# Kernel tuning notes

Hardware: AMD Instinct MI355X
Metric: run time of the kernel (lower is better)

The kernel has to match this reference:

```python
import jax, jax.numpy as jnp
import numpy as np

BETA = 4.0  # temperature of soft cluster assignment in filling loss


def _pairwise_sq_dist(a, b):
    # a: [N,D], b: [K,D] -> [N,K] squared euclidean distances
    return (jnp.sum(a * a, -1, keepdims=True)
            - 2.0 * (a @ b.T)
            + jnp.sum(b * b, -1)[None, :])


def setup_inputs() -> dict:
    key = jax.random.key(0)
    k1, k2, k3, k4 = jax.random.split(key, 4)
    N, D, K = 131072, 64, 16
    x = jax.random.normal(k1, (N, D), jnp.float32)
    cluster_centers = jax.random.normal(k2, (K, D), jnp.float32)
    target = jax.random.normal(k3, (N, D), jnp.float32)
    ft = jax.random.uniform(k4, (K,), jnp.float32)
    filling_target = ft / ft.sum()
    # prediction = kmeans assignment of the fixed target set (computed once, constant)
    prediction = jnp.argmin(_pairwise_sq_dist(target, cluster_centers), axis=-1)
    return {"x": x, "cluster_centers": cluster_centers,
            "filling_target": filling_target, "target": target,
            "prediction": prediction}


def reference(x, cluster_centers, filling_target, target, prediction):
    N, D = x.shape
    Nt = target.shape[0]
    K = cluster_centers.shape[0]
    BIG = jnp.finfo(x.dtype).max  # padding value that sorts to the end

    d2 = _pairwise_sq_dist(x, cluster_centers)  # [N,K]

    # --- cluster filling MSE: soft assignment fractions vs filling_target ---
    soft = jax.nn.softmax(-BETA * d2, axis=-1)          # [N,K]
    filling = soft.mean(axis=0)                          # [K]
    loss_fil = jnp.mean((filling - filling_target) ** 2)

    # --- per-cluster sorted (per-dimension 1D) Wasserstein distance ---
    pred_x = jax.lax.stop_gradient(jnp.argmin(d2, axis=-1))  # kmeans_predict(x).detach()
    L = min(N, Nt)  # static upper bound on per-cluster min_size
    rows = jnp.arange(L)

    loss_med = jnp.zeros((), x.dtype)
    for k in range(K):  # fixed structural loop over clusters
        mx = pred_x == k
        mt = prediction == k
        m = jnp.minimum(mx.sum(), mt.sum())  # min_size (dynamic value, static shapes)
        # keep only the FIRST m members (original order), as x[in_cluster][:m]
        keep_x = mx & ((jnp.cumsum(mx) - 1) < m)
        keep_t = mt & ((jnp.cumsum(mt) - 1) < m)
        # mask out non-members with BIG so they sort to the bottom, sort per dim
        xs = jnp.sort(jnp.where(keep_x[:, None], x, BIG), axis=0)[:L]       # [L,D]
        ts = jnp.sort(jnp.where(keep_t[:, None], target, BIG), axis=0)[:L]  # [L,D]
        valid = (rows < m)[:, None]                                          # [L,1]
        diff = jnp.where(valid, jnp.abs(xs - ts), 0.0)
        # mean(|sort(x) - sort(y)|) over the m x D selected elements
        denom = (m * D).astype(x.dtype)
        loss_med = loss_med + jnp.where(m > 0, diff.sum() / denom, 0.0)

    return loss_fil + loss_med
```

## Files before the change

### kernel.cpp

```cpp
#include <hip/hip_runtime.h>
#include <stdint.h>

#define N_ROWS 131072
#define DIMS 64
#define KCL 16
#define BETA 4.0f
#define NBLK 512
#define LCH 8192
#define LST 512
#define SEG_STRIDE 263168
#define VOFF (1u<<21)

typedef unsigned long long u64;
typedef unsigned int u32;

__device__ __forceinline__ u32 enc_f(float f) {
  u32 u = __float_as_uint(f);
  return (u & 0x80000000u) ? ~u : (u | 0x80000000u);
}
__device__ __forceinline__ float dec_f(u32 e) {
  u32 u = (e & 0x80000000u) ? (e & 0x7FFFFFFFu) : ~e;
  return __uint_as_float(u);
}
__device__ __forceinline__ u32 U4(u32 u) { return u ^ ((u >> 3) & 7u); }

#define CS(a,b,dd) { u32 _mn = min(a,b), _mx = max(a,b); a = (dd)?_mn:_mx; b = (dd)?_mx:_mn; }
#define CSV(A,B,D) { CS(A.x,B.x,D) CS(A.y,B.y,D) CS(A.z,B.z,D) CS(A.w,B.w,D) }

#define M16G(a,b,c,d,e,f,g,h,i2,j2,k2,l,m,n,o,p,D) \
  CS(a,i2,D) CS(b,j2,D) CS(c,k2,D) CS(d,l,D) CS(e,m,D) CS(f,n,D) CS(g,o,D) CS(h,p,D) \
  CS(a,e,D)  CS(b,f,D)  CS(c,g,D)  CS(d,h,D) CS(i2,m,D) CS(j2,n,D) CS(k2,o,D) CS(l,p,D) \
  CS(a,c,D)  CS(b,d,D)  CS(e,g,D)  CS(f,h,D) CS(i2,k2,D) CS(j2,l,D) CS(m,o,D) CS(n,p,D) \
  CS(a,b,D)  CS(c,d,D)  CS(e,f,D)  CS(g,h,D) CS(i2,j2,D) CS(k2,l,D) CS(m,n,D) CS(o,p,D)

#define SORT16G(a,b,c,d,e,f,g,h,i2,j2,k2,l,m,n,o,p,D) \
  CS(a,b,D) CS(c,d,!(D)) CS(e,f,D) CS(g,h,!(D)) CS(i2,j2,D) CS(k2,l,!(D)) CS(m,n,D) CS(o,p,!(D)) \
  CS(a,c,D) CS(b,d,D) CS(e,g,!(D)) CS(f,h,!(D)) CS(i2,k2,D) CS(j2,l,D) CS(m,o,!(D)) CS(n,p,!(D)) \
  CS(a,b,D) CS(c,d,D) CS(e,f,!(D)) CS(g,h,!(D)) CS(i2,j2,D) CS(k2,l,D) CS(m,n,!(D)) CS(o,p,!(D)) \
  CS(a,e,D) CS(b,f,D) CS(c,g,D) CS(d,h,D) CS(i2,m,!(D)) CS(j2,n,!(D)) CS(k2,o,!(D)) CS(l,p,!(D)) \
  CS(a,c,D) CS(b,d,D) CS(e,g,D) CS(f,h,D) CS(i2,k2,!(D)) CS(j2,l,!(D)) CS(m,o,!(D)) CS(n,p,!(D)) \
  CS(a,b,D) CS(c,d,D) CS(e,f,D) CS(g,h,D) CS(i2,j2,!(D)) CS(k2,l,!(D)) CS(m,n,!(D)) CS(o,p,!(D)) \
  M16G(a,b,c,d,e,f,g,h,i2,j2,k2,l,m,n,o,p,D)

#define MERGE16F(D) M16G(r0,r1,r2,r3,r4,r5,r6,r7,r8,r9,r10,r11,r12,r13,r14,r15,D)
#define SORT16F(D)  SORT16G(r0,r1,r2,r3,r4,r5,r6,r7,r8,r9,r10,r11,r12,r13,r14,r15,D)

#define LOADTILE16(src) \
  { uint4 _a0=src[U4(ub+0)],_a1=src[U4(ub+1)],_a2=src[U4(ub+2)],_a3=src[U4(ub+3)]; \
    r0=_a0.x;r1=_a0.y;r2=_a0.z;r3=_a0.w; r4=_a1.x;r5=_a1.y;r6=_a1.z;r7=_a1.w; \
    r8=_a2.x;r9=_a2.y;r10=_a2.z;r11=_a2.w; r12=_a3.x;r13=_a3.y;r14=_a3.z;r15=_a3.w; }

#define STORETILE16(dst) \
  { dst[U4(ub+0)]=make_uint4(r0,r1,r2,r3);   dst[U4(ub+1)]=make_uint4(r4,r5,r6,r7); \
    dst[U4(ub+2)]=make_uint4(r8,r9,r10,r11); dst[U4(ub+3)]=make_uint4(r12,r13,r14,r15); }

__device__ __forceinline__ void wave_tail(uint4* lds4, u32 RU, u32 Lw, u32 gbase,
                                          u32 k, u32 jtop, u32 lane)
{
  u32 j = jtop;
  while (j >= 32u) {
    u32 ud = j >> 3;
    if (lane < (Lw >> 4)) {
      u32 bu = RU + (((lane & ~(ud - 1u)) << 2) | (lane & (ud - 1u)));
      bool up = (((gbase + (bu << 2)) & k) == 0u);
      uint4 A0 = lds4[U4(bu)],           A1 = lds4[U4(bu + ud)],
            A2 = lds4[U4(bu + 2u * ud)], A3 = lds4[U4(bu + 3u * ud)];
      CSV(A0,A2,up) CSV(A1,A3,up)
      CSV(A0,A1,up) CSV(A2,A3,up)
      lds4[U4(bu)] = A0;           lds4[U4(bu + ud)] = A1;
      lds4[U4(bu + 2u * ud)] = A2; lds4[U4(bu + 3u * ud)] = A3;
    }
    j >>= 2;
  }
  if (j == 16u) {
    u32 total = Lw >> 3;
    for (u32 inst = lane; inst < total; inst += 64u) {
      u32 bu = RU + (((inst & ~3u) << 1) | (inst & 3u));
      bool up = (((gbase + (bu << 2)) & k) == 0u);
      uint4 A = lds4[U4(bu)], B = lds4[U4(bu + 4u)];
      CSV(A,B,up)
      lds4[U4(bu)] = A; lds4[U4(bu + 4u)] = B;
    }
  }
}

__device__ __forceinline__ void block_cross(uint4* lds4, u32 Wn, u32 gbase,
                                            u32 k, u32 jtop, u32 tid)
{
  if (jtop == 1024u) {
    u32 total = Wn >> 3;
    for (u32 inst = tid; inst < total; inst += LST) {
      u32 bu = ((inst & ~255u) << 1) | (inst & 255u);
      bool up = (((gbase + (bu << 2)) & k) == 0u);
      uint4 A = lds4[U4(bu)], B = lds4[U4(bu + 256u)];
      CSV(A,B,up)
      lds4[U4(bu)] = A; lds4[U4(bu + 256u)] = B;
    }
  } else if (jtop == 2048u) {
    u32 total = Wn >> 4;
    for (u32 inst = tid; inst < total; inst += LST) {
      u32 bu = ((inst & ~255u) << 2) | (inst & 255u);
      bool up = (((gbase + (bu << 2)) & k) == 0u);
      uint4 A0 = lds4[U4(bu)],         A1 = lds4[U4(bu + 256u)],
            A2 = lds4[U4(bu + 512u)],  A3 = lds4[U4(bu + 768u)];
      CSV(A0,A2,up) CSV(A1,A3,up)
      CSV(A0,A1,up) CSV(A2,A3,up)
      lds4[U4(bu)] = A0;        lds4[U4(bu + 256u)] = A1;
      lds4[U4(bu + 512u)] = A2; lds4[U4(bu + 768u)] = A3;
    }
  } else {
    u32 total = Wn >> 5;
    for (u32 inst = tid; inst < total; inst += LST) {
      u32 bu = ((inst & ~255u) << 3) | (inst & 255u);
      bool up = (((gbase + (bu << 2)) & k) == 0u);
      uint4 A0 = lds4[U4(bu)],          A1 = lds4[U4(bu + 256u)],
            A2 = lds4[U4(bu + 512u)],   A3 = lds4[U4(bu + 768u)],
            A4 = lds4[U4(bu + 1024u)],  A5 = lds4[U4(bu + 1280u)],
            A6 = lds4[U4(bu + 1536u)],  A7 = lds4[U4(bu + 1792u)];
      CSV(A0,A4,up) CSV(A1,A5,up) CSV(A2,A6,up) CSV(A3,A7,up)
      CSV(A0,A2,up) CSV(A1,A3,up) CSV(A4,A6,up) CSV(A5,A7,up)
      CSV(A0,A1,up) CSV(A2,A3,up) CSV(A4,A5,up) CSV(A6,A7,up)
      lds4[U4(bu)] = A0;         lds4[U4(bu + 256u)] = A1;
      lds4[U4(bu + 512u)] = A2;  lds4[U4(bu + 768u)] = A3;
      lds4[U4(bu + 1024u)] = A4; lds4[U4(bu + 1280u)] = A5;
      lds4[U4(bu + 1536u)] = A6; lds4[U4(bu + 1792u)] = A7;
    }
  }
}

__global__ __launch_bounds__(256) void k_assign(
    const float* __restrict__ x, const float* __restrict__ centers,
    const int* __restrict__ predT, int* __restrict__ predX,
    float* __restrict__ fill_sum, u32* __restrict__ histX, u32* __restrict__ histT)
{
  __shared__ float c[KCL][DIMS];
  __shared__ float cn[KCL];
  __shared__ float fs[KCL];
  __shared__ u32 hx[KCL], ht[KCL];
  int tid = threadIdx.x;
  for (int t = tid; t < KCL * DIMS; t += 256) c[t / DIMS][t % DIMS] = centers[t];
  if (tid < KCL) { fs[tid] = 0.f; hx[tid] = 0; ht[tid] = 0; }
  __syncthreads();
  if (tid < KCL) {
    float s = 0.f;
    for (int d = 0; d < DIMS; ++d) s += c[tid][d] * c[tid][d];
    cn[tid] = s;
  }
  __syncthreads();
  int i = blockIdx.x * 256 + tid;
  const float4* xr = (const float4*)(x + (size_t)i * DIMS);
  float dot[KCL];
#pragma unroll
  for (int k = 0; k < KCL; ++k) dot[k] = 0.f;
  for (int t = 0; t < DIMS / 4; ++t) {
    float4 v = xr[t];
#pragma unroll
    for (int k = 0; k < KCL; ++k)
      dot[k] += v.x * c[k][4 * t] + v.y * c[k][4 * t + 1] + v.z * c[k][4 * t + 2] + v.w * c[k][4 * t + 3];
  }
  float sc[KCL];
  float smin = 3.0e38f; int kmin = 0;
#pragma unroll
  for (int k = 0; k < KCL; ++k) {
    sc[k] = cn[k] - 2.f * dot[k];
    if (sc[k] < smin) { smin = sc[k]; kmin = k; }
  }
  float e[KCL]; float esum = 0.f;
#pragma unroll
  for (int k = 0; k < KCL; ++k) { e[k] = expf(-BETA * (sc[k] - smin)); esum += e[k]; }
  float inv = 1.f / esum;
#pragma unroll
  for (int k = 0; k < KCL; ++k) atomicAdd(&fs[k], e[k] * inv);
  predX[i] = kmin;
  atomicAdd(&hx[kmin], 1u);
  atomicAdd(&ht[predT[i]], 1u);
  __syncthreads();
  if (tid < KCL) {
    histX[blockIdx.x * KCL + tid] = hx[tid];
    histT[blockIdx.x * KCL + tid] = ht[tid];
    atomicAdd(&fill_sum[tid], fs[tid]);
  }
}

__global__ __launch_bounds__(512) void k_scan(
    const u32* __restrict__ histX, const u32* __restrict__ histT,
    u32* __restrict__ baseX, u32* __restrict__ baseT,
    const float* __restrict__ fill_sum, const float* __restrict__ ftarget,
    int* __restrict__ m_out, float* __restrict__ w_out,
    int* __restrict__ p_out, int* __restrict__ pOff_out, int* __restrict__ padOff_out,
    int* __restrict__ nlo_out, float* __restrict__ loss_fil)
{
  __shared__ u32 part[2][KCL][17];
  __shared__ u32 tot[2][KCL];
  __shared__ float sq[KCL];
  __shared__ int sp[KCL];
  __shared__ int smv[KCL];
  int tid = threadIdx.x;
  int side = tid >> 8;
  int rem = tid & 255;
  int c = rem >> 4;
  int sub = rem & 15;
  const u32* hist = side ? histT : histX;
  u32* base = side ? baseT : baseX;
  int b0 = sub * 32;
  u32 s = 0;
  for (int b = b0; b < b0 + 32; ++b) s += hist[b * KCL + c];
  part[side][c][sub] = s;
  __syncthreads();
  if (sub == 0) {
    u32 run = 0;
    for (int t = 0; t < 16; ++t) { u32 v = part[side][c][t]; part[side][c][t] = run; run += v; }
    tot[side][c] = run;
  }
  __syncthreads();
  u32 run = part[side][c][sub];
  for (int b = b0; b < b0 + 32; ++b) { base[b * KCL + c] = run; run += hist[b * KCL + c]; }
  if (tid < KCL) {
    int m = min((int)tot[0][tid], (int)tot[1][tid]);
    m_out[tid] = m;
    smv[tid] = m;
    w_out[tid] = (m > 0) ? 1.f / ((float)m * (float)DIMS) : 0.f;
    int pp = 32;
    while (pp < m) pp <<= 1;
    sp[tid] = pp;
    p_out[tid] = pp;
    int nlo = 0;
    if (pp > LCH) {
      int nch = pp / LCH;
      for (int j = 1; j < nch; j += 2) {
        int v = m - j * LCH;
        if (v < 0) v = 0;
        if (v > LCH) v = LCH;
        nlo += LCH - v;
      }
    }
    nlo_out[tid] = nlo;
    float d = fill_sum[tid] / (float)N_ROWS - ftarget[tid];
    sq[tid] = d * d;
  }
  __syncthreads();
  if (tid == 0) {
    float s2 = 0.f;
    int acc = 0, pacc = 0;
    for (int k = 0; k < KCL; ++k) {
      s2 += sq[k];
      pOff_out[k] = acc;
      acc += sp[k];
      padOff_out[k] = pacc;
      pacc += sp[k] - smv[k];
    }
    pOff_out[KCL] = acc;
    padOff_out[KCL] = pacc;
    *loss_fil = s2 / (float)KCL;
  }
}

__global__ __launch_bounds__(256) void k_rank(
    const int* __restrict__ predX, const int* __restrict__ predT,
    const u32* __restrict__ baseX, const u32* __restrict__ baseT,
    const int* __restrict__ m, int* __restrict__ rankX, int* __restrict__ rankT)
{
  __shared__ int wcX[4][KCL], wcT[4][KCL];
  int tid = threadIdx.x;
  int lane = tid & 63, wave = tid >> 6;
  int i = blockIdx.x * 256 + tid;
  int kx = predX[i], kt = predT[i];
  u64 below = (1ull << lane) - 1ull;
  int lrX = 0, lrT = 0;
  for (int cc = 0; cc < KCL; ++cc) {
    u64 mx = __ballot(kx == cc);
    u64 mt = __ballot(kt == cc);
    if (kx == cc) lrX = __popcll(mx & below);
    if (kt == cc) lrT = __popcll(mt & below);
    if (lane == 0) { wcX[wave][cc] = __popcll(mx); wcT[wave][cc] = __popcll(mt); }
  }
  __syncthreads();
  int wbX = 0, wbT = 0;
  for (int w2 = 0; w2 < wave; ++w2) { wbX += wcX[w2][kx]; wbT += wcT[w2][kt]; }
  int rX = (int)baseX[blockIdx.x * KCL + kx] + wbX + lrX;
  int rT = (int)baseT[blockIdx.x * KCL + kt] + wbT + lrT;
  rankX[i] = (rX < m[kx]) ? rX : -1;
  rankT[i] = (rT < m[kt]) ? rT : -1;
}

__global__ __launch_bounds__(256) void k_pad(
    u32* __restrict__ vbase, const int* __restrict__ pOffG,
    const int* __restrict__ padOffG, const int* __restrict__ mG,
    const int* __restrict__ pG)
{
  __shared__ int sOff[KCL];
  __shared__ int sPad[KCL + 1];
  __shared__ int sM[KCL];
  __shared__ int sP[KCL];
  int tid = threadIdx.x;
  if (tid < KCL) { sOff[tid] = pOffG[tid]; sM[tid] = mG[tid]; sP[tid] = pG[tid]; }
  if (tid <= KCL) sPad[tid] = padOffG[tid];
  __syncthreads();
  int tot = sPad[KCL];
  u32* seg = vbase + (size_t)blockIdx.y * SEG_STRIDE;
  for (int tt = blockIdx.x * 256 + tid; tt < tot; tt += gridDim.x * 256) {
    int c = 0;
#pragma unroll
    for (int cc = 1; cc < KCL; ++cc) c += (tt >= sPad[cc]) ? 1 : 0;
    int local = sM[c] + (tt - sPad[c]);
    u32 val = (sP[c] > LCH && ((local >> 13) & 1)) ? 0u : 0xFFFFFFFFu;
    seg[sOff[c] + local] = val;
  }
}

__global__ __launch_bounds__(256) void k_scatter(
    const float* __restrict__ x, const float* __restrict__ tgt,
    const int* __restrict__ predX, const int* __restrict__ predT,
    const int* __restrict__ rankX, const int* __restrict__ rankT,
    const int* __restrict__ pOffG,
    u32* __restrict__ valX, u32* __restrict__ valT, int d0, int Dbc)
{
  __shared__ int spOff[KCL + 1];
  int tid = threadIdx.x;
  if (tid <= KCL) spOff[tid] = pOffG[tid];
  __syncthreads();
  int i = blockIdx.x * 256 + tid;
  int cx = predX[i], rx = rankX[i];
  int ct = predT[i], rt = rankT[i];
  bool vec = ((Dbc & 3) == 0);
  if (rx >= 0) {
    size_t pos = (size_t)spOff[cx] + rx;
    const float* xr = x + (size_t)i * DIMS + d0;
    if (vec) {
      const float4* x4 = (const float4*)xr;
      for (int d = 0; d < Dbc; d += 4) {
        float4 v = x4[d >> 2];
        valX[(size_t)(d + 0) * SEG_STRIDE + pos] = enc_f(v.x);
        valX[(size_t)(d + 1) * SEG_STRIDE + pos] = enc_f(v.y);
        valX[(size_t)(d + 2) * SEG_STRIDE + pos] = enc_f(v.z);
        valX[(size_t)(d + 3) * SEG_STRIDE + pos] = enc_f(v.w);
      }
    } else {
      for (int d = 0; d < Dbc; ++d) valX[(size_t)d * SEG_STRIDE + pos] = enc_f(xr[d]);
    }
  }
  if (rt >= 0) {
    size_t pos = (size_t)spOff[ct] + rt;
    const float* tr = tgt + (size_t)i * DIMS + d0;
    if (vec) {
      const float4* t4 = (const float4*)tr;
      for (int d = 0; d < Dbc; d += 4) {
        float4 v = t4[d >> 2];
        valT[(size_t)(d + 0) * SEG_STRIDE + pos] = enc_f(v.x);
        valT[(size_t)(d + 1) * SEG_STRIDE + pos] = enc_f(v.y);
        valT[(size_t)(d + 2) * SEG_STRIDE + pos] = enc_f(v.z);
        valT[(size_t)(d + 3) * SEG_STRIDE + pos] = enc_f(v.w);
      }
    } else {
      for (int d = 0; d < Dbc; ++d) valT[(size_t)d * SEG_STRIDE + pos] = enc_f(tr[d]);
    }
  }
}

__global__ __launch_bounds__(LST, 8) void k_local_sort(
    u32* __restrict__ vbase, const int* __restrict__ pG, const int* __restrict__ pOffG,
    const int* __restrict__ mG)
{
  __shared__ __align__(16) u32 lds[LCH];
  uint4* lds4 = (uint4*)lds;
  int t = blockIdx.x, c = -1, sub = 0, acc = 0;
  for (int cc = 0; cc < KCL; ++cc) {
    int pc0 = pG[cc];
    int nc = (pc0 > LCH) ? (pc0 / LCH) : 1;
    if (t < acc + nc) { c = cc; sub = t - acc; break; }
    acc += nc;
  }
  if (c < 0) return;
  int pc = pG[c];
  u32 CH = (u32)min(pc, LCH);
  u32 gb = (u32)sub * (u32)LCH;
  int v = mG[c] - (int)gb;
  if (v > (int)CH) v = (int)CH;
  if (v <= 0) return;
  u32 W = 32u;
  while (W < (u32)v) W <<= 1;
  if (W > CH) W = CH;
  bool desc = (pc > LCH) && (sub & 1);
  u32 inv = desc ? 0xFFFFFFFFu : 0u;
  u32* seg = vbase + (size_t)blockIdx.y * SEG_STRIDE + pOffG[c] + gb;
  uint4* gp4 = (uint4*)seg;
  u32 tid = threadIdx.x;
  u32 lane = tid & 63u;
  u32 wv = tid >> 6;
  u32 ub = tid << 2;
  u32 bas = tid << 4;
  bool act = (bas < W);
  u32 RU = wv << 8;
  u32 runBase = wv << 10;
  bool wact = (runBase < W);
  u32 Lw = W - runBase; if (Lw > 1024u) Lw = 1024u;
  u32 r0,r1,r2,r3,r4,r5,r6,r7,r8,r9,r10,r11,r12,r13,r14,r15;

  if (act) {
    uint4 a0 = gp4[ub + 0], a1 = gp4[ub + 1], a2 = gp4[ub + 2], a3 = gp4[ub + 3];
    r0 = a0.x^inv; r1 = a0.y^inv; r2  = a0.z^inv; r3  = a0.w^inv;
    r4 = a1.x^inv; r5 = a1.y^inv; r6  = a1.z^inv; r7  = a1.w^inv;
    r8 = a2.x^inv; r9 = a2.y^inv; r10 = a2.z^inv; r11 = a2.w^inv;
    r12 = a3.x^inv; r13 = a3.y^inv; r14 = a3.z^inv; r15 = a3.w^inv;
    bool D = ((bas & 16u) == 0u);
    SORT16F(D);
    STORETILE16(lds4);
  }
  if (wact) {
    for (u32 k = 32u; k <= Lw; k <<= 1) {
      wave_tail(lds4, RU, Lw, 0u, k, k >> 1, lane);
      if (act) {
        LOADTILE16(lds4);
        bool D = ((bas & k) == 0u);
        MERGE16F(D);
        if (k < W) { STORETILE16(lds4); }
        else {
          gp4[ub + 0] = make_uint4(r0^inv, r1^inv, r2^inv, r3^inv);
          gp4[ub + 1] = make_uint4(r4^inv, r5^inv, r6^inv, r7^inv);
          gp4[ub + 2] = make_uint4(r8^inv, r9^inv, r10^inv, r11^inv);
          gp4[ub + 3] = make_uint4(r12^inv, r13^inv, r14^inv, r15^inv);
        }
      }
    }
  }

  if (W >= 2048u) {
    __syncthreads();
    for (u32 k = 2048u; k <= W; k <<= 1) {
      block_cross(lds4, W, 0u, k, k >> 1, tid);
      __syncthreads();
      if (wact) {
        wave_tail(lds4, RU, Lw, 0u, k, 512u, lane);
        if (act) {
          LOADTILE16(lds4);
          bool D = ((bas & k) == 0u);
          MERGE16F(D);
          if (k < W) { STORETILE16(lds4); }
          else {
            gp4[ub + 0] = make_uint4(r0^inv, r1^inv, r2^inv, r3^inv);
            gp4[ub + 1] = make_uint4(r4^inv, r5^inv, r6^inv, r7^inv);
            gp4[ub + 2] = make_uint4(r8^inv, r9^inv, r10^inv, r11^inv);
            gp4[ub + 3] = make_uint4(r12^inv, r13^inv, r14^inv, r15^inv);
          }
        }
      }
      if (k < W) __syncthreads();
    }
  }
}

__global__ __launch_bounds__(256) void k_gpass(
    u32* __restrict__ vbase, const int* __restrict__ pG, const int* __restrict__ pOffG,
    int kk, int j)
{
  u32* base = vbase + (size_t)blockIdx.y * SEG_STRIDE;
  int pb[KCL]; int tot = 0;
#pragma unroll
  for (int c = 0; c < KCL; ++c) {
    pb[c] = tot;
    int pc = pG[c];
    if (pc >= kk) tot += pc >> 1;
  }
  for (int g4 = (blockIdx.x * 256 + threadIdx.x) << 2; g4 < tot; g4 += gridDim.x * 256 * 4) {
    int c = 0;
#pragma unroll
    for (int cc = 1; cc < KCL; ++cc) c += (g4 >= pb[cc]) ? 1 : 0;
    int u = g4 - pb[c];
    int i = ((u & ~(j - 1)) << 1) | (u & (j - 1));
    bool up = ((i & kk) == 0);
    u32* s2 = base + pOffG[c];
    uint4 A = *(const uint4*)(s2 + i);
    uint4 B = *(const uint4*)(s2 + i + j);
    CS(A.x, B.x, up) CS(A.y, B.y, up) CS(A.z, B.z, up) CS(A.w, B.w, up)
    *(uint4*)(s2 + i) = A;
    *(uint4*)(s2 + i + j) = B;
  }
}

__global__ __launch_bounds__(LST, 8) void k_gfinish(
    u32* __restrict__ vbase, const int* __restrict__ pG, const int* __restrict__ pOffG, int kk)
{
  __shared__ __align__(16) u32 lds[LCH];
  uint4* lds4 = (uint4*)lds;
  int t = blockIdx.x, c = -1, sub = 0, acc = 0;
  for (int cc = 0; cc < KCL; ++cc) {
    int pc = pG[cc];
    if (pc < kk) continue;
    int nc = pc / LCH;
    if (t < acc + nc) { c = cc; sub = t - acc; break; }
    acc += nc;
  }
  if (c < 0) return;
  u32 gb = (u32)sub * (u32)LCH;
  u32* seg = vbase + (size_t)blockIdx.y * SEG_STRIDE + pOffG[c] + gb;
  uint4* gp4 = (uint4*)seg;
  u32 tid = threadIdx.x;
  u32 lane = tid & 63u;
  u32 wv = tid >> 6;
  u32 RU = wv << 8;
  u32 ub = tid << 2;
  u32 bas = tid << 4;
  u32 r0,r1,r2,r3,r4,r5,r6,r7,r8,r9,r10,r11,r12,r13,r14,r15;

  for (u32 uu = tid; uu < LCH / 4; uu += LST) lds4[U4(uu)] = gp4[uu];
  __syncthreads();
  block_cross(lds4, (u32)LCH, gb, (u32)kk, 4096u, tid);
  __syncthreads();
  wave_tail(lds4, RU, 1024u, gb, (u32)kk, 512u, lane);
  {
    LOADTILE16(lds4);
    bool up = (((gb + bas) & (u32)kk) == 0u);
    MERGE16F(up);
    gp4[ub + 0] = make_uint4(r0, r1, r2, r3);
    gp4[ub + 1] = make_uint4(r4, r5, r6, r7);
    gp4[ub + 2] = make_uint4(r8, r9, r10, r11);
    gp4[ub + 3] = make_uint4(r12, r13, r14, r15);
  }
}

__global__ __launch_bounds__(256) void k_reduce(
    const u32* __restrict__ valX, const u32* __restrict__ valT,
    const int* __restrict__ pOffG, const int* __restrict__ mG,
    const int* __restrict__ nloG,
    const float* __restrict__ wG, float* __restrict__ lossAcc, int Dbc)
{
  __shared__ int spOff[KCL + 1];
  __shared__ int sm[KCL];
  __shared__ int snlo[KCL];
  __shared__ float swt[KCL];
  __shared__ float red[256];
  int tid = threadIdx.x;
  if (tid <= KCL) spOff[tid] = pOffG[tid];
  if (tid < KCL) { sm[tid] = mG[tid]; snlo[tid] = nloG[tid]; swt[tid] = wG[tid]; }
  __syncthreads();
  int d = blockIdx.y;
  const u32* vx = valX + (size_t)d * SEG_STRIDE;
  const u32* vt = valT + (size_t)d * SEG_STRIDE;
  int P16 = spOff[KCL];
  float s = 0.f;
  for (int pos = blockIdx.x * 256 + tid; pos < P16; pos += gridDim.x * 256) {
    int c = 0;
#pragma unroll
    for (int cc = 1; cc < KCL; ++cc) c += (pos >= spOff[cc]) ? 1 : 0;
    int rel = pos - spOff[c] - snlo[c];
    if ((unsigned)rel < (unsigned)sm[c]) {
      float a = dec_f(vx[pos]), b = dec_f(vt[pos]);
      s += fabsf(a - b) * swt[c];
    }
  }
  red[tid] = s;
  __syncthreads();
  for (int st = 128; st > 0; st >>= 1) {
    if (tid < st) red[tid] += red[tid + st];
    __syncthreads();
  }
  if (tid == 0) atomicAdd(lossAcc, red[0]);
}

__global__ void k_final(const float* __restrict__ lossAcc, const float* __restrict__ loss_fil,
                        float* __restrict__ out)
{
  out[0] = *lossAcc + *loss_fil;
}

extern "C" void kernel_launch(void* const* d_in, const int* in_sizes, int n_in,
                              void* d_out, int out_size, void* d_ws, size_t ws_size,
                              hipStream_t stream)
{
  const float* x       = (const float*)d_in[0];
  const float* centers = (const float*)d_in[1];
  const float* ftarget = (const float*)d_in[2];
  const float* tgt     = (const float*)d_in[3];
  const int*   predT   = (const int*)d_in[4];
  float* out = (float*)d_out;

  char* ws = (char*)d_ws;
  float* fill_sum = (float*)(ws + 0);
  float* lossAcc  = (float*)(ws + 64);
  float* loss_fil = (float*)(ws + 68);
  int*   m_buf    = (int*)(ws + 128);
  float* w_buf    = (float*)(ws + 192);
  int*   p_buf    = (int*)(ws + 256);
  int*   pOff     = (int*)(ws + 320);
  int*   padOff   = (int*)(ws + 400);
  u32* histX = (u32*)(ws + 512);
  u32* histT = (u32*)(ws + 512 + 32768);
  u32* baseX = (u32*)(ws + 512 + 65536);
  u32* baseT = (u32*)(ws + 512 + 98304);
  int* predX = (int*)(ws + 131584);
  int* rankX = (int*)(ws + 655872);
  int* rankT = (int*)(ws + 1180160);
  int* nlo_buf = (int*)(ws + 1704448);
  u32* vbase = (u32*)(ws + VOFF);

  size_t avail_elems = (ws_size > VOFF) ? ((ws_size - VOFF) / 4) : 0;
  int Db = (int)(avail_elems / (2ull * SEG_STRIDE));
  if (Db > DIMS) Db = DIMS;
  if (Db >= 4) Db &= ~3;
  if (Db < 1) Db = 1;

  hipMemsetAsync(ws, 0, 128, stream);
  k_assign<<<NBLK, 256, 0, stream>>>(x, centers, predT, predX, fill_sum, histX, histT);
  k_scan<<<1, 512, 0, stream>>>(histX, histT, baseX, baseT, fill_sum, ftarget,
                                m_buf, w_buf, p_buf, pOff, padOff, nlo_buf, loss_fil);
  k_rank<<<NBLK, 256, 0, stream>>>(predX, predT, baseX, baseT, m_buf, rankX, rankT);

  for (int d0 = 0; d0 < DIMS; d0 += Db) {
    int Dbc = (Db < DIMS - d0) ? Db : (DIMS - d0);
    u32* valX = vbase;
    u32* valT = vbase + (size_t)Dbc * SEG_STRIDE;
    k_pad<<<dim3(16, 2 * Dbc), 256, 0, stream>>>(vbase, pOff, padOff, m_buf, p_buf);
    k_scatter<<<NBLK, 256, 0, stream>>>(x, tgt, predX, predT, rankX, rankT, pOff,
                                        valX, valT, d0, Dbc);
    k_local_sort<<<dim3(40, 2 * Dbc), LST, 0, stream>>>(vbase, p_buf, pOff, m_buf);
    for (int kk = 2 * LCH; kk <= N_ROWS; kk <<= 1) {
      int gx = (kk == 2 * LCH) ? 32 : 8;
      for (int j = kk >> 1; j >= LCH; j >>= 1)
        k_gpass<<<dim3(gx, 2 * Dbc), 256, 0, stream>>>(vbase, p_buf, pOff, kk, j);
      k_gfinish<<<dim3(32, 2 * Dbc), LST, 0, stream>>>(vbase, p_buf, pOff, kk);
    }
    k_reduce<<<dim3(32, Dbc), 256, 0, stream>>>(valX, valT, pOff, m_buf, nlo_buf,
                                                w_buf, lossAcc, Dbc);
  }
  k_final<<<1, 1, 0, stream>>>(lossAcc, loss_fil, out);
}
```

Measured before the change: 740.8 us.

## Double sort chunk size, fuse padding into gather, compact reduce over valid elements

Doubles the in-LDS bitonic chunk to 16384 elements with 1024-thread blocks, which cuts the number of global merge passes and kernel launches. The pad and scatter kernels are replaced by a rank kernel that writes compacted index lists and one gather kernel that writes both the values and the padding sentinels. The reduce kernel now iterates only over valid elements through prefix offsets instead of testing every padded position. The larger LDS footprint per block may lower occupancy, and the gather reads rows of x in an irregular order.

```diff
diff --git a/kernel.cpp b/kernel.cpp
--- a/kernel.cpp
+++ b/kernel.cpp
@@ -6,8 +6,8 @@
 #define KCL 16
 #define BETA 4.0f
 #define NBLK 512
-#define LCH 8192
-#define LST 512
+#define CHUNK 16384
+#define STH 1024
 #define SEG_STRIDE 263168
 #define VOFF (1u<<21)
 
@@ -84,47 +84,51 @@
   }
 }
 
-__device__ __forceinline__ void block_cross(uint4* lds4, u32 Wn, u32 gbase,
-                                            u32 k, u32 jtop, u32 tid)
-{
-  if (jtop == 1024u) {
-    u32 total = Wn >> 3;
-    for (u32 inst = tid; inst < total; inst += LST) {
-      u32 bu = ((inst & ~255u) << 1) | (inst & 255u);
-      bool up = (((gbase + (bu << 2)) & k) == 0u);
-      uint4 A = lds4[U4(bu)], B = lds4[U4(bu + 256u)];
-      CSV(A,B,up)
-      lds4[U4(bu)] = A; lds4[U4(bu + 256u)] = B;
-    }
-  } else if (jtop == 2048u) {
-    u32 total = Wn >> 4;
-    for (u32 inst = tid; inst < total; inst += LST) {
-      u32 bu = ((inst & ~255u) << 2) | (inst & 255u);
-      bool up = (((gbase + (bu << 2)) & k) == 0u);
-      uint4 A0 = lds4[U4(bu)],         A1 = lds4[U4(bu + 256u)],
-            A2 = lds4[U4(bu + 512u)],  A3 = lds4[U4(bu + 768u)];
-      CSV(A0,A2,up) CSV(A1,A3,up)
-      CSV(A0,A1,up) CSV(A2,A3,up)
-      lds4[U4(bu)] = A0;        lds4[U4(bu + 256u)] = A1;
-      lds4[U4(bu + 512u)] = A2; lds4[U4(bu + 768u)] = A3;
-    }
-  } else {
-    u32 total = Wn >> 5;
-    for (u32 inst = tid; inst < total; inst += LST) {
-      u32 bu = ((inst & ~255u) << 3) | (inst & 255u);
-      bool up = (((gbase + (bu << 2)) & k) == 0u);
-      uint4 A0 = lds4[U4(bu)],          A1 = lds4[U4(bu + 256u)],
-            A2 = lds4[U4(bu + 512u)],   A3 = lds4[U4(bu + 768u)],
-            A4 = lds4[U4(bu + 1024u)],  A5 = lds4[U4(bu + 1280u)],
-            A6 = lds4[U4(bu + 1536u)],  A7 = lds4[U4(bu + 1792u)];
-      CSV(A0,A4,up) CSV(A1,A5,up) CSV(A2,A6,up) CSV(A3,A7,up)
-      CSV(A0,A2,up) CSV(A1,A3,up) CSV(A4,A6,up) CSV(A5,A7,up)
-      CSV(A0,A1,up) CSV(A2,A3,up) CSV(A4,A5,up) CSV(A6,A7,up)
-      lds4[U4(bu)] = A0;         lds4[U4(bu + 256u)] = A1;
-      lds4[U4(bu + 512u)] = A2;  lds4[U4(bu + 768u)] = A3;
-      lds4[U4(bu + 1024u)] = A4; lds4[U4(bu + 1280u)] = A5;
-      lds4[U4(bu + 1536u)] = A6; lds4[U4(bu + 1792u)] = A7;
-    }
+__device__ __forceinline__ void cross1(uint4* lds4, u32 Wn, u32 gb, u32 k, u32 jtop, u32 tid)
+{
+  u32 ud = jtop >> 2;
+  u32 total = Wn >> 3;
+  for (u32 inst = tid; inst < total; inst += STH) {
+    u32 bu = ((inst & ~(ud - 1u)) << 1) | (inst & (ud - 1u));
+    bool up = (((gb + (bu << 2)) & k) == 0u);
+    uint4 A = lds4[U4(bu)], B = lds4[U4(bu + ud)];
+    CSV(A,B,up)
+    lds4[U4(bu)] = A; lds4[U4(bu + ud)] = B;
+  }
+}
+__device__ __forceinline__ void cross2(uint4* lds4, u32 Wn, u32 gb, u32 k, u32 jtop, u32 tid)
+{
+  u32 ud = jtop >> 3;
+  u32 total = Wn >> 4;
+  for (u32 inst = tid; inst < total; inst += STH) {
+    u32 bu = ((inst & ~(ud - 1u)) << 2) | (inst & (ud - 1u));
+    bool up = (((gb + (bu << 2)) & k) == 0u);
+    uint4 A0 = lds4[U4(bu)],            A1 = lds4[U4(bu + ud)],
+          A2 = lds4[U4(bu + 2u * ud)],  A3 = lds4[U4(bu + 3u * ud)];
+    CSV(A0,A2,up) CSV(A1,A3,up)
+    CSV(A0,A1,up) CSV(A2,A3,up)
+    lds4[U4(bu)] = A0;           lds4[U4(bu + ud)] = A1;
+    lds4[U4(bu + 2u * ud)] = A2; lds4[U4(bu + 3u * ud)] = A3;
+  }
+}
+__device__ __forceinline__ void cross3(uint4* lds4, u32 Wn, u32 gb, u32 k, u32 jtop, u32 tid)
+{
+  u32 ud = jtop >> 4;
+  u32 total = Wn >> 5;
+  for (u32 inst = tid; inst < total; inst += STH) {
+    u32 bu = ((inst & ~(ud - 1u)) << 3) | (inst & (ud - 1u));
+    bool up = (((gb + (bu << 2)) & k) == 0u);
+    uint4 A0 = lds4[U4(bu)],            A1 = lds4[U4(bu + ud)],
+          A2 = lds4[U4(bu + 2u * ud)],  A3 = lds4[U4(bu + 3u * ud)],
+          A4 = lds4[U4(bu + 4u * ud)],  A5 = lds4[U4(bu + 5u * ud)],
+          A6 = lds4[U4(bu + 6u * ud)],  A7 = lds4[U4(bu + 7u * ud)];
+    CSV(A0,A4,up) CSV(A1,A5,up) CSV(A2,A6,up) CSV(A3,A7,up)
+    CSV(A0,A2,up) CSV(A1,A3,up) CSV(A4,A6,up) CSV(A5,A7,up)
+    CSV(A0,A1,up) CSV(A2,A3,up) CSV(A4,A5,up) CSV(A6,A7,up)
+    lds4[U4(bu)] = A0;           lds4[U4(bu + ud)] = A1;
+    lds4[U4(bu + 2u * ud)] = A2; lds4[U4(bu + 3u * ud)] = A3;
+    lds4[U4(bu + 4u * ud)] = A4; lds4[U4(bu + 5u * ud)] = A5;
+    lds4[U4(bu + 6u * ud)] = A6; lds4[U4(bu + 7u * ud)] = A7;
   }
 }
 
@@ -187,7 +191,7 @@
     u32* __restrict__ baseX, u32* __restrict__ baseT,
     const float* __restrict__ fill_sum, const float* __restrict__ ftarget,
     int* __restrict__ m_out, float* __restrict__ w_out,
-    int* __restrict__ p_out, int* __restrict__ pOff_out, int* __restrict__ padOff_out,
+    int* __restrict__ p_out, int* __restrict__ pOff_out, int* __restrict__ mOff_out,
     int* __restrict__ nlo_out, float* __restrict__ loss_fil)
 {
   __shared__ u32 part[2][KCL][17];
@@ -225,13 +229,13 @@
     sp[tid] = pp;
     p_out[tid] = pp;
     int nlo = 0;
-    if (pp > LCH) {
-      int nch = pp / LCH;
+    if (pp > CHUNK) {
+      int nch = pp / CHUNK;
       for (int j = 1; j < nch; j += 2) {
-        int v = m - j * LCH;
+        int v = m - j * CHUNK;
         if (v < 0) v = 0;
-        if (v > LCH) v = LCH;
-        nlo += LCH - v;
+        if (v > CHUNK) v = CHUNK;
+        nlo += CHUNK - v;
       }
     }
     nlo_out[tid] = nlo;
@@ -241,16 +245,16 @@
   __syncthreads();
   if (tid == 0) {
     float s2 = 0.f;
-    int acc = 0, pacc = 0;
+    int acc = 0, macc = 0;
     for (int k = 0; k < KCL; ++k) {
       s2 += sq[k];
       pOff_out[k] = acc;
       acc += sp[k];
-      padOff_out[k] = pacc;
-      pacc += sp[k] - smv[k];
+      mOff_out[k] = macc;
+      macc += smv[k];
     }
     pOff_out[KCL] = acc;
-    padOff_out[KCL] = pacc;
+    mOff_out[KCL] = macc;
     *loss_fil = s2 / (float)KCL;
   }
 }
@@ -258,11 +262,14 @@
 __global__ __launch_bounds__(256) void k_rank(
     const int* __restrict__ predX, const int* __restrict__ predT,
     const u32* __restrict__ baseX, const u32* __restrict__ baseT,
-    const int* __restrict__ m, int* __restrict__ rankX, int* __restrict__ rankT)
+    const int* __restrict__ mG, const int* __restrict__ mOffG,
+    int* __restrict__ idxX, int* __restrict__ idxT)
 {
   __shared__ int wcX[4][KCL], wcT[4][KCL];
+  __shared__ int smo[KCL], sm2[KCL];
   int tid = threadIdx.x;
   int lane = tid & 63, wave = tid >> 6;
+  if (tid < KCL) { smo[tid] = mOffG[tid]; sm2[tid] = mG[tid]; }
   int i = blockIdx.x * 256 + tid;
   int kx = predX[i], kt = predT[i];
   u64 below = (1ull << lane) - 1ull;
@@ -279,108 +286,91 @@
   for (int w2 = 0; w2 < wave; ++w2) { wbX += wcX[w2][kx]; wbT += wcT[w2][kt]; }
   int rX = (int)baseX[blockIdx.x * KCL + kx] + wbX + lrX;
   int rT = (int)baseT[blockIdx.x * KCL + kt] + wbT + lrT;
-  rankX[i] = (rX < m[kx]) ? rX : -1;
-  rankT[i] = (rT < m[kt]) ? rT : -1;
-}
-
-__global__ __launch_bounds__(256) void k_pad(
-    u32* __restrict__ vbase, const int* __restrict__ pOffG,
-    const int* __restrict__ padOffG, const int* __restrict__ mG,
-    const int* __restrict__ pG)
-{
-  __shared__ int sOff[KCL];
-  __shared__ int sPad[KCL + 1];
-  __shared__ int sM[KCL];
-  __shared__ int sP[KCL];
-  int tid = threadIdx.x;
-  if (tid < KCL) { sOff[tid] = pOffG[tid]; sM[tid] = mG[tid]; sP[tid] = pG[tid]; }
-  if (tid <= KCL) sPad[tid] = padOffG[tid];
-  __syncthreads();
-  int tot = sPad[KCL];
-  u32* seg = vbase + (size_t)blockIdx.y * SEG_STRIDE;
-  for (int tt = blockIdx.x * 256 + tid; tt < tot; tt += gridDim.x * 256) {
-    int c = 0;
-#pragma unroll
-    for (int cc = 1; cc < KCL; ++cc) c += (tt >= sPad[cc]) ? 1 : 0;
-    int local = sM[c] + (tt - sPad[c]);
-    u32 val = (sP[c] > LCH && ((local >> 13) & 1)) ? 0u : 0xFFFFFFFFu;
-    seg[sOff[c] + local] = val;
-  }
-}
-
-__global__ __launch_bounds__(256) void k_scatter(
+  if (rX < sm2[kx]) idxX[smo[kx] + rX] = i;
+  if (rT < sm2[kt]) idxT[smo[kt] + rT] = i;
+}
+
+__global__ __launch_bounds__(256) void k_gather(
     const float* __restrict__ x, const float* __restrict__ tgt,
-    const int* __restrict__ predX, const int* __restrict__ predT,
-    const int* __restrict__ rankX, const int* __restrict__ rankT,
-    const int* __restrict__ pOffG,
+    const int* __restrict__ idxX, const int* __restrict__ idxT,
+    const int* __restrict__ pOffG, const int* __restrict__ mOffG,
+    const int* __restrict__ mG, const int* __restrict__ pG,
     u32* __restrict__ valX, u32* __restrict__ valT, int d0, int Dbc)
 {
   __shared__ int spOff[KCL + 1];
+  __shared__ int smo[KCL], sm2[KCL], sp2[KCL];
   int tid = threadIdx.x;
   if (tid <= KCL) spOff[tid] = pOffG[tid];
-  __syncthreads();
-  int i = blockIdx.x * 256 + tid;
-  int cx = predX[i], rx = rankX[i];
-  int ct = predT[i], rt = rankT[i];
-  bool vec = ((Dbc & 3) == 0);
-  if (rx >= 0) {
-    size_t pos = (size_t)spOff[cx] + rx;
-    const float* xr = x + (size_t)i * DIMS + d0;
-    if (vec) {
-      const float4* x4 = (const float4*)xr;
-      for (int d = 0; d < Dbc; d += 4) {
-        float4 v = x4[d >> 2];
-        valX[(size_t)(d + 0) * SEG_STRIDE + pos] = enc_f(v.x);
-        valX[(size_t)(d + 1) * SEG_STRIDE + pos] = enc_f(v.y);
-        valX[(size_t)(d + 2) * SEG_STRIDE + pos] = enc_f(v.z);
-        valX[(size_t)(d + 3) * SEG_STRIDE + pos] = enc_f(v.w);
+  if (tid < KCL) { smo[tid] = mOffG[tid]; sm2[tid] = mG[tid]; sp2[tid] = pG[tid]; }
+  __syncthreads();
+  int pos = blockIdx.x * 256 + tid;
+  if (pos >= spOff[KCL]) return;
+  int c = 0;
+#pragma unroll
+  for (int cc = 1; cc < KCL; ++cc) c += (pos >= spOff[cc]) ? 1 : 0;
+  int rel = pos - spOff[c];
+  u32* dx = valX + pos;
+  u32* dt = valT + pos;
+  if (rel < sm2[c]) {
+    int w = smo[c] + rel;
+    int iX = idxX[w], iT = idxT[w];
+    if ((Dbc & 3) == 0) {
+      const float4* xr = (const float4*)(x + (size_t)iX * DIMS + d0);
+      const float4* tr = (const float4*)(tgt + (size_t)iT * DIMS + d0);
+      for (int q = 0; q < (Dbc >> 2); ++q) {
+        float4 a = xr[q];
+        float4 b = tr[q];
+        size_t base = (size_t)(4 * q) * SEG_STRIDE;
+        dx[base]                  = enc_f(a.x);
+        dx[base + SEG_STRIDE]     = enc_f(a.y);
+        dx[base + 2 * (size_t)SEG_STRIDE] = enc_f(a.z);
+        dx[base + 3 * (size_t)SEG_STRIDE] = enc_f(a.w);
+        dt[base]                  = enc_f(b.x);
+        dt[base + SEG_STRIDE]     = enc_f(b.y);
+        dt[base + 2 * (size_t)SEG_STRIDE] = enc_f(b.z);
+        dt[base + 3 * (size_t)SEG_STRIDE] = enc_f(b.w);
       }
     } else {
-      for (int d = 0; d < Dbc; ++d) valX[(size_t)d * SEG_STRIDE + pos] = enc_f(xr[d]);
-    }
-  }
-  if (rt >= 0) {
-    size_t pos = (size_t)spOff[ct] + rt;
-    const float* tr = tgt + (size_t)i * DIMS + d0;
-    if (vec) {
-      const float4* t4 = (const float4*)tr;
-      for (int d = 0; d < Dbc; d += 4) {
-        float4 v = t4[d >> 2];
-        valT[(size_t)(d + 0) * SEG_STRIDE + pos] = enc_f(v.x);
-        valT[(size_t)(d + 1) * SEG_STRIDE + pos] = enc_f(v.y);
-        valT[(size_t)(d + 2) * SEG_STRIDE + pos] = enc_f(v.z);
-        valT[(size_t)(d + 3) * SEG_STRIDE + pos] = enc_f(v.w);
+      const float* xr = x + (size_t)iX * DIMS + d0;
+      const float* tr = tgt + (size_t)iT * DIMS + d0;
+      for (int d = 0; d < Dbc; ++d) {
+        dx[(size_t)d * SEG_STRIDE] = enc_f(xr[d]);
+        dt[(size_t)d * SEG_STRIDE] = enc_f(tr[d]);
       }
-    } else {
-      for (int d = 0; d < Dbc; ++d) valT[(size_t)d * SEG_STRIDE + pos] = enc_f(tr[d]);
-    }
-  }
-}
-
-__global__ __launch_bounds__(LST, 8) void k_local_sort(
+    }
+  } else {
+    u32 pv = (sp2[c] > CHUNK && ((rel >> 14) & 1)) ? 0u : 0xFFFFFFFFu;
+    for (int d = 0; d < Dbc; ++d) {
+      dx[(size_t)d * SEG_STRIDE] = pv;
+      dt[(size_t)d * SEG_STRIDE] = pv;
+    }
+  }
+}
+
+__global__ __launch_bounds__(STH, 8) void k_sort(
     u32* __restrict__ vbase, const int* __restrict__ pG, const int* __restrict__ pOffG,
     const int* __restrict__ mG)
 {
-  __shared__ __align__(16) u32 lds[LCH];
+  __shared__ __align__(16) u32 lds[CHUNK];
   uint4* lds4 = (uint4*)lds;
   int t = blockIdx.x, c = -1, sub = 0, acc = 0;
   for (int cc = 0; cc < KCL; ++cc) {
     int pc0 = pG[cc];
-    int nc = (pc0 > LCH) ? (pc0 / LCH) : 1;
+    int nc = (pc0 > CHUNK) ? (pc0 / CHUNK) : 1;
     if (t < acc + nc) { c = cc; sub = t - acc; break; }
     acc += nc;
   }
   if (c < 0) return;
   int pc = pG[c];
-  u32 CH = (u32)min(pc, LCH);
-  u32 gb = (u32)sub * (u32)LCH;
+  u32 CH = (u32)min(pc, CHUNK);
+  u32 gb = (u32)sub * (u32)CHUNK;
   int v = mG[c] - (int)gb;
   if (v > (int)CH) v = (int)CH;
   if (v <= 0) return;
   u32 W = 32u;
   while (W < (u32)v) W <<= 1;
   if (W > CH) W = CH;
-  bool desc = (pc > LCH) && (sub & 1);
+  bool desc = (pc > CHUNK) && (sub & 1);
   u32 inv = desc ? 0xFFFFFFFFu : 0u;
   u32* seg = vbase + (size_t)blockIdx.y * SEG_STRIDE + pOffG[c] + gb;
   uint4* gp4 = (uint4*)seg;
@@ -427,8 +417,22 @@
   if (W >= 2048u) {
     __syncthreads();
     for (u32 k = 2048u; k <= W; k <<= 1) {
-      block_cross(lds4, W, 0u, k, k >> 1, tid);
-      __syncthreads();
+      u32 jt = k >> 1;
+      if (jt >= 8192u) {
+        cross3(lds4, W, 0u, k, 8192u, tid);
+        __syncthreads();
+        cross1(lds4, W, 0u, k, 1024u, tid);
+        __syncthreads();
+      } else if (jt == 4096u) {
+        cross3(lds4, W, 0u, k, 4096u, tid);
+        __syncthreads();
+      } else if (jt == 2048u) {
+        cross2(lds4, W, 0u, k, 2048u, tid);
+        __syncthreads();
+      } else {
+        cross1(lds4, W, 0u, k, 1024u, tid);
+        __syncthreads();
+      }
       if (wact) {
         wave_tail(lds4, RU, Lw, 0u, k, 512u, lane);
         if (act) {
@@ -477,21 +481,21 @@
   }
 }
 
-__global__ __launch_bounds__(LST, 8) void k_gfinish(
+__global__ __launch_bounds__(STH, 8) void k_gfinish(
     u32* __restrict__ vbase, const int* __restrict__ pG, const int* __restrict__ pOffG, int kk)
 {
-  __shared__ __align__(16) u32 lds[LCH];
+  __shared__ __align__(16) u32 lds[CHUNK];
   uint4* lds4 = (uint4*)lds;
   int t = blockIdx.x, c = -1, sub = 0, acc = 0;
   for (int cc = 0; cc < KCL; ++cc) {
     int pc = pG[cc];
     if (pc < kk) continue;
-    int nc = pc / LCH;
+    int nc = pc / CHUNK;
     if (t < acc + nc) { c = cc; sub = t - acc; break; }
     acc += nc;
   }
   if (c < 0) return;
-  u32 gb = (u32)sub * (u32)LCH;
+  u32 gb = (u32)sub * (u32)CHUNK;
   u32* seg = vbase + (size_t)blockIdx.y * SEG_STRIDE + pOffG[c] + gb;
   uint4* gp4 = (uint4*)seg;
   u32 tid = threadIdx.x;
@@ -502,9 +506,11 @@
   u32 bas = tid << 4;
   u32 r0,r1,r2,r3,r4,r5,r6,r7,r8,r9,r10,r11,r12,r13,r14,r15;
 
-  for (u32 uu = tid; uu < LCH / 4; uu += LST) lds4[U4(uu)] = gp4[uu];
-  __syncthreads();
-  block_cross(lds4, (u32)LCH, gb, (u32)kk, 4096u, tid);
+  for (u32 uu = tid; uu < CHUNK / 4; uu += STH) lds4[U4(uu)] = gp4[uu];
+  __syncthreads();
+  cross3(lds4, (u32)CHUNK, gb, (u32)kk, 8192u, tid);
+  __syncthreads();
+  cross1(lds4, (u32)CHUNK, gb, (u32)kk, 1024u, tid);
   __syncthreads();
   wave_tail(lds4, RU, 1024u, gb, (u32)kk, 512u, lane);
   {
@@ -520,33 +526,31 @@
 
 __global__ __launch_bounds__(256) void k_reduce(
     const u32* __restrict__ valX, const u32* __restrict__ valT,
-    const int* __restrict__ pOffG, const int* __restrict__ mG,
+    const int* __restrict__ pOffG, const int* __restrict__ mOffG,
     const int* __restrict__ nloG,
-    const float* __restrict__ wG, float* __restrict__ lossAcc, int Dbc)
-{
-  __shared__ int spOff[KCL + 1];
-  __shared__ int sm[KCL];
+    const float* __restrict__ wG, float* __restrict__ lossAcc)
+{
+  __shared__ int spOff[KCL];
+  __shared__ int smo[KCL + 1];
   __shared__ int snlo[KCL];
   __shared__ float swt[KCL];
   __shared__ float red[256];
   int tid = threadIdx.x;
-  if (tid <= KCL) spOff[tid] = pOffG[tid];
-  if (tid < KCL) { sm[tid] = mG[tid]; snlo[tid] = nloG[tid]; swt[tid] = wG[tid]; }
+  if (tid <= KCL) smo[tid] = mOffG[tid];
+  if (tid < KCL) { spOff[tid] = pOffG[tid]; snlo[tid] = nloG[tid]; swt[tid] = wG[tid]; }
   __syncthreads();
   int d = blockIdx.y;
   const u32* vx = valX + (size_t)d * SEG_STRIDE;
   const u32* vt = valT + (size_t)d * SEG_STRIDE;
-  int P16 = spOff[KCL];
+  int M = smo[KCL];
   float s = 0.f;
-  for (int pos = blockIdx.x * 256 + tid; pos < P16; pos += gridDim.x * 256) {
+  for (int w = blockIdx.x * 256 + tid; w < M; w += gridDim.x * 256) {
     int c = 0;
 #pragma unroll
-    for (int cc = 1; cc < KCL; ++cc) c += (pos >= spOff[cc]) ? 1 : 0;
-    int rel = pos - spOff[c] - snlo[c];
-    if ((unsigned)rel < (unsigned)sm[c]) {
-      float a = dec_f(vx[pos]), b = dec_f(vt[pos]);
-      s += fabsf(a - b) * swt[c];
-    }
+    for (int cc = 1; cc < KCL; ++cc) c += (w >= smo[cc]) ? 1 : 0;
+    int pos = spOff[c] + snlo[c] + (w - smo[c]);
+    float a = dec_f(vx[pos]), b = dec_f(vt[pos]);
+    s += fabsf(a - b) * swt[c];
   }
   red[tid] = s;
   __syncthreads();
@@ -582,14 +586,14 @@
   float* w_buf    = (float*)(ws + 192);
   int*   p_buf    = (int*)(ws + 256);
   int*   pOff     = (int*)(ws + 320);
-  int*   padOff   = (int*)(ws + 400);
+  int*   mOff     = (int*)(ws + 400);
   u32* histX = (u32*)(ws + 512);
   u32* histT = (u32*)(ws + 512 + 32768);
   u32* baseX = (u32*)(ws + 512 + 65536);
   u32* baseT = (u32*)(ws + 512 + 98304);
   int* predX = (int*)(ws + 131584);
-  int* rankX = (int*)(ws + 655872);
-  int* rankT = (int*)(ws + 1180160);
+  int* idxX  = (int*)(ws + 655872);
+  int* idxT  = (int*)(ws + 1180160);
   int* nlo_buf = (int*)(ws + 1704448);
   u32* vbase = (u32*)(ws + VOFF);
 
@@ -602,25 +606,23 @@
   hipMemsetAsync(ws, 0, 128, stream);
   k_assign<<<NBLK, 256, 0, stream>>>(x, centers, predT, predX, fill_sum, histX, histT);
   k_scan<<<1, 512, 0, stream>>>(histX, histT, baseX, baseT, fill_sum, ftarget,
-                                m_buf, w_buf, p_buf, pOff, padOff, nlo_buf, loss_fil);
-  k_rank<<<NBLK, 256, 0, stream>>>(predX, predT, baseX, baseT, m_buf, rankX, rankT);
+                                m_buf, w_buf, p_buf, pOff, mOff, nlo_buf, loss_fil);
+  k_rank<<<NBLK, 256, 0, stream>>>(predX, predT, baseX, baseT, m_buf, mOff, idxX, idxT);
 
   for (int d0 = 0; d0 < DIMS; d0 += Db) {
     int Dbc = (Db < DIMS - d0) ? Db : (DIMS - d0);
     u32* valX = vbase;
     u32* valT = vbase + (size_t)Dbc * SEG_STRIDE;
-    k_pad<<<dim3(16, 2 * Dbc), 256, 0, stream>>>(vbase, pOff, padOff, m_buf, p_buf);
-    k_scatter<<<NBLK, 256, 0, stream>>>(x, tgt, predX, predT, rankX, rankT, pOff,
-                                        valX, valT, d0, Dbc);
-    k_local_sort<<<dim3(40, 2 * Dbc), LST, 0, stream>>>(vbase, p_buf, pOff, m_buf);
-    for (int kk = 2 * LCH; kk <= N_ROWS; kk <<= 1) {
-      int gx = (kk == 2 * LCH) ? 32 : 8;
-      for (int j = kk >> 1; j >= LCH; j >>= 1)
-        k_gpass<<<dim3(gx, 2 * Dbc), 256, 0, stream>>>(vbase, p_buf, pOff, kk, j);
-      k_gfinish<<<dim3(32, 2 * Dbc), LST, 0, stream>>>(vbase, p_buf, pOff, kk);
-    }
-    k_reduce<<<dim3(32, Dbc), 256, 0, stream>>>(valX, valT, pOff, m_buf, nlo_buf,
-                                                w_buf, lossAcc, Dbc);
+    k_gather<<<1028, 256, 0, stream>>>(x, tgt, idxX, idxT, pOff, mOff, m_buf, p_buf,
+                                       valX, valT, d0, Dbc);
+    k_sort<<<dim3(26, 2 * Dbc), STH, 0, stream>>>(vbase, p_buf, pOff, m_buf);
+    for (int kk = 2 * CHUNK; kk <= N_ROWS; kk <<= 1) {
+      for (int j = kk >> 1; j >= CHUNK; j >>= 1)
+        k_gpass<<<dim3(16, 2 * Dbc), 256, 0, stream>>>(vbase, p_buf, pOff, kk, j);
+      k_gfinish<<<dim3(16, 2 * Dbc), STH, 0, stream>>>(vbase, p_buf, pOff, kk);
+    }
+    k_reduce<<<dim3(32, Dbc), 256, 0, stream>>>(valX, valT, pOff, mOff, nlo_buf,
+                                                w_buf, lossAcc);
   }
   k_final<<<1, 1, 0, stream>>>(lossAcc, loss_fil, out);
 }
```

Measured after the change: 652.8 us. 11.9% less time.
